# Performance work log

Measured on AMD Instinct MI355X. Metric: run time of the kernel, lower is better.

The kernel has to match this reference:

```python
import jax, jax.numpy as jnp
import numpy as np

B, S, E, H, FF = 4, 2048, 512, 8, 2048
DH = E // H
EPS = 1e-6


def setup_inputs() -> dict:
    key = jax.random.key(0)
    ks = jax.random.split(key, 16)
    sc = lambda fan_in: 1.0 / np.sqrt(fan_in)
    inp = {
        "x": jax.random.normal(ks[0], (B, S, E), dtype=jnp.float32),
        "src_mask": jnp.ones((B, 1, 1, S), dtype=jnp.int32),
        # attention projections, stored [in, out]
        "wq": jax.random.uniform(ks[1], (E, E), minval=-sc(E), maxval=sc(E)),
        "bq": jnp.zeros((E,), jnp.float32),
        "wk": jax.random.uniform(ks[2], (E, E), minval=-sc(E), maxval=sc(E)),
        "bk": jnp.zeros((E,), jnp.float32),
        "wv": jax.random.uniform(ks[3], (E, E), minval=-sc(E), maxval=sc(E)),
        "bv": jnp.zeros((E,), jnp.float32),
        "wo": jax.random.uniform(ks[4], (E, E), minval=-sc(E), maxval=sc(E)),
        "bo": jnp.zeros((E,), jnp.float32),
        # feed-forward
        "w1": jax.random.uniform(ks[5], (E, FF), minval=-sc(E), maxval=sc(E)),
        "b1": jnp.zeros((FF,), jnp.float32),
        "w2": jax.random.uniform(ks[6], (FF, E), minval=-sc(FF), maxval=sc(FF)),
        "b2": jnp.zeros((E,), jnp.float32),
        # addNormLayer scalar params (alpha init 1, bias init 0)
        "alpha1": jnp.ones((1,), jnp.float32),
        "beta1": jnp.zeros((1,), jnp.float32),
        "alpha2": jnp.ones((1,), jnp.float32),
        "beta2": jnp.zeros((1,), jnp.float32),
    }
    return inp


def _norm(x, alpha, beta):
    # matches torch: mean + unbiased std (ddof=1), eps added to std
    mean = jnp.mean(x, axis=-1, keepdims=True)
    std = jnp.std(x, axis=-1, keepdims=True, ddof=1)
    return alpha * (x - mean) / (std + EPS) + beta


def reference(x, src_mask, wq, bq, wk, bk, wv, bv, wo, bo,
              w1, b1, w2, b2, alpha1, beta1, alpha2, beta2):
    # --- residual 1: pre-norm self-attention ---
    n = _norm(x, alpha1, beta1)  # [B,S,E]
    q = (n @ wq + bq).reshape(B, S, H, DH).transpose(0, 2, 1, 3)  # [B,H,S,DH]
    k = (n @ wk + bk).reshape(B, S, H, DH).transpose(0, 2, 1, 3)
    v = (n @ wv + bv).reshape(B, S, H, DH).transpose(0, 2, 1, 3)
    scores = jnp.einsum('bhqd,bhkd->bhqk', q, k) / np.sqrt(DH)  # [B,H,S,S]
    scores = jnp.where(src_mask == 0, -1e9, scores)
    attn = jax.nn.softmax(scores, axis=-1)
    ctx = jnp.einsum('bhqk,bhkd->bhqd', attn, v)  # [B,H,S,DH]
    ctx = ctx.transpose(0, 2, 1, 3).reshape(B, S, E)
    x = x + (ctx @ wo + bo)
    # --- residual 2: pre-norm FFN ---
    n2 = _norm(x, alpha2, beta2)
    ff = jax.nn.relu(n2 @ w1 + b1) @ w2 + b2
    return x + ff
```

## Files before the change

### kernel.cpp

```cpp
#include <hip/hip_runtime.h>

typedef __bf16 bfrag __attribute__((ext_vector_type(8)));
typedef float f32x4 __attribute__((ext_vector_type(4)));
typedef unsigned short us8 __attribute__((ext_vector_type(8)));

__device__ __forceinline__ float bf2f(unsigned short s) {
  unsigned u = ((unsigned)s) << 16;
  float f;
  __builtin_memcpy(&f, &u, 4);
  return f;
}
__device__ __forceinline__ unsigned short f2bf(float f) {
  unsigned u;
  __builtin_memcpy(&u, &f, 4);
  u += 0x7fffu + ((u >> 16) & 1u);
  return (unsigned short)(u >> 16);
}
__device__ __forceinline__ float rdf(const void* p, size_t i, int isf) {
  return isf ? ((const float*)p)[i] : bf2f(((const unsigned short*)p)[i]);
}
__device__ __forceinline__ void gld16(const unsigned short* g, unsigned short* l) {
  __builtin_amdgcn_global_load_lds(
      (const __attribute__((address_space(1))) unsigned int*)g,
      (__attribute__((address_space(3))) unsigned int*)l, 16, 0, 0);
}

template <int XMODE>
__device__ void norm_unit(const void* xin, const void* alpha, const void* beta,
                          unsigned short* out, int isf, int u) {
  constexpr int E = 512;
  int xf = XMODE ? 1 : isf;
  int tid = threadIdx.x;
  int wave = tid >> 6, lane = tid & 63;
  size_t tok = (size_t)u * 4 + wave;
  float v[8];
  if (xf) {
    const float* xp = (const float*)xin + tok * E + lane * 8;
    float4 a0 = *(const float4*)xp;
    float4 a1 = *(const float4*)(xp + 4);
    v[0] = a0.x; v[1] = a0.y; v[2] = a0.z; v[3] = a0.w;
    v[4] = a1.x; v[5] = a1.y; v[6] = a1.z; v[7] = a1.w;
  } else {
    us8 uu = *(const us8*)((const unsigned short*)xin + tok * E + lane * 8);
#pragma unroll
    for (int j = 0; j < 8; j++) v[j] = bf2f(uu[j]);
  }
  float s = 0.f, sq = 0.f;
#pragma unroll
  for (int j = 0; j < 8; j++) { s += v[j]; sq += v[j] * v[j]; }
#pragma unroll
  for (int off = 1; off < 64; off <<= 1) {
    s += __shfl_xor(s, off, 64);
    sq += __shfl_xor(sq, off, 64);
  }
  float mean = s * (1.0f / 512.0f);
  float var = fmaxf((sq - 512.0f * mean * mean) * (1.0f / 511.0f), 0.0f);
  float inv = rdf(alpha, 0, isf) / (sqrtf(var) + 1e-6f);
  float be = rdf(beta, 0, isf);
  us8 ov;
#pragma unroll
  for (int j = 0; j < 8; j++) ov[j] = f2bf((v[j] - mean) * inv + be);
  *(us8*)(out + tok * E + lane * 8) = ov;
}

__global__ __launch_bounds__(256) void setup_k(
    const unsigned short* __restrict__ x16,
    const void* wq, const void* wk, const void* wv, const void* wo,
    const void* w1, const void* w2,
    unsigned short* wqkvT, unsigned short* woT,
    unsigned short* w1T, unsigned short* w2T,
    const void* bq, const void* bk, const void* bv, const void* bo,
    const void* b1, const void* b2, float* __restrict__ bcat,
    const void* alpha1, const void* beta1, unsigned short* __restrict__ n1,
    int* __restrict__ flag) {
  __shared__ unsigned short tile[32][33];
  __shared__ int s_cnt;
  int tid = threadIdx.x;
  int bid = blockIdx.x;
  if (tid == 0) s_cnt = 0;
  __syncthreads();
  {
    int c = 0;
    for (int i = tid; i < 4096; i += 256) {
      unsigned short s = x16[2 * i];
      int e = (s >> 7) & 0xFF;
      if (e > 0xC2 || (e != 0 && e < 0x3D)) c++;
    }
    atomicAdd(&s_cnt, c);
  }
  __syncthreads();
  const int isf = (s_cnt > 256) ? 1 : 0;
  if (bid == 0 && tid == 0) flag[0] = isf;

  if (bid >= 3090) {
    norm_unit<0>(x16, alpha1, beta1, n1, isf, bid - 3090);
    return;
  }
  if (bid >= 3072) {
    int i = (bid - 3072) * 256 + tid;
    if (i < 4608) {
      float v;
      if (i < 512) v = rdf(bq, i, isf);
      else if (i < 1024) v = rdf(bk, i - 512, isf);
      else if (i < 1536) v = rdf(bv, i - 1024, isf);
      else if (i < 2048) v = rdf(bo, i - 1536, isf);
      else if (i < 4096) v = rdf(b1, i - 2048, isf);
      else v = rdf(b2, i - 4096, isf);
      bcat[i] = v;
    }
    return;
  }
  const void* W;
  unsigned short* Wt;
  int K, N, t;
  if (bid < 1024) {
    K = 512; N = 512; t = bid & 255;
    if (bid < 256) { W = wq; Wt = wqkvT; }
    else if (bid < 512) { W = wk; Wt = wqkvT + 262144; }
    else if (bid < 768) { W = wv; Wt = wqkvT + 524288; }
    else { W = wo; Wt = woT; }
  } else if (bid < 2048) {
    W = w1; Wt = w1T; K = 512; N = 2048; t = bid - 1024;
  } else {
    W = w2; Wt = w2T; K = 2048; N = 512; t = bid - 2048;
  }
  int nx = N >> 5;
  int n0 = (t % nx) * 32, k0 = (t / nx) * 32;
#pragma unroll
  for (int i = 0; i < 4; i++) {
    int e = tid + i * 256;
    int r = e >> 5, c = e & 31;
    tile[r][c] = f2bf(rdf(W, (size_t)(k0 + r) * N + n0 + c, isf));
  }
  __syncthreads();
#pragma unroll
  for (int i = 0; i < 4; i++) {
    int e = tid + i * 256;
    int r = e >> 5, c = e & 31;
    Wt[(size_t)(n0 + r) * K + k0 + c] = tile[c][r];
  }
}

__global__ __launch_bounds__(256) void vtrans_k(
    const unsigned short* __restrict__ qkb, unsigned short* __restrict__ vbt) {
  __shared__ unsigned short tile[32][33];
  int tid = threadIdx.x;
  int u = blockIdx.x;
  int s0 = (u & 63) * 32;
  int d0 = ((u >> 6) & 1) * 32;
  int bh = u >> 7, b = bh >> 3, h = bh & 7;
#pragma unroll
  for (int i = 0; i < 4; i++) {
    int e = tid + i * 256;
    int r = e >> 5, c = e & 31;
    tile[r][c] = qkb[((size_t)b * 2048 + s0 + r) * 1536 + 1024 + h * 64 + d0 + c];
  }
  __syncthreads();
#pragma unroll
  for (int i = 0; i < 4; i++) {
    int e = tid + i * 256;
    int r = e >> 5, c = e & 31;
    vbt[((size_t)bh * 64 + d0 + r) * 2048 + s0 + c] = tile[c][r];
  }
}

__global__ __launch_bounds__(256) void norm2_k(
    const void* __restrict__ xin, const void* __restrict__ alpha,
    const void* __restrict__ beta, unsigned short* __restrict__ out,
    const int* __restrict__ flag) {
  norm_unit<1>(xin, alpha, beta, out, flag[0], blockIdx.x);
}

template <int TN, int RES, int OUTM, int RELU>
__global__ __launch_bounds__(256, 3) void gemm2_k(
    const unsigned short* __restrict__ A,
    const unsigned short* __restrict__ Bt,
    const float* __restrict__ bias,
    const void* __restrict__ res,
    void* __restrict__ outp,
    int N, int K, const int* __restrict__ flag) {
  constexpr int MT = (TN == 128) ? 4 : 2;
  constexpr int BROWS = TN / 4;
  __shared__ alignas(16) unsigned short As[128 * 64];
  __shared__ alignas(16) unsigned short Bs[TN * 64];
  int isf = flag[0];
  int outf32 = (OUTM == 1) || (OUTM == 2 && isf);
  int tid = threadIdx.x;
  int wave = tid >> 6, lane = tid & 63;
  int quad = lane >> 4, l16 = lane & 15, l7 = l16 & 7;
  int wm = (TN == 128) ? (wave >> 1) : wave;
  int wn = (TN == 128) ? (wave & 1) : 0;
  size_t m0 = (size_t)blockIdx.x * 128;
  size_t n0 = (size_t)blockIdx.y * TN;

  int lrow = lane >> 3;
  int gcol = 8 * ((lane & 7) ^ lrow);

  const unsigned short* ag = A + (m0 + wave * 32 + lrow) * K + gcol;
  const unsigned short* bg = Bt + (n0 + wave * BROWS + lrow) * K + gcol;
  unsigned short* asl = &As[(wave * 32) * 64];
  unsigned short* bsl = &Bs[(wave * BROWS) * 64];

  f32x4 acc[MT][4];
#pragma unroll
  for (int i = 0; i < MT; i++)
#pragma unroll
    for (int j = 0; j < 4; j++) acc[i][j] = {0.f, 0.f, 0.f, 0.f};

  for (int k0 = 0; k0 < K; k0 += 64) {
    __syncthreads();
#pragma unroll
    for (int c = 0; c < 4; c++)
      gld16(ag + (size_t)(8 * c) * K + k0, asl + (8 * c) * 64);
#pragma unroll
    for (int c = 0; c < BROWS / 8; c++)
      gld16(bg + (size_t)(8 * c) * K + k0, bsl + (8 * c) * 64);
    __syncthreads();
#pragma unroll
    for (int ko = 0; ko < 2; ko++) {
      int slot = ((4 * ko + quad) ^ l7) * 8;
      bfrag af[MT], bf[4];
#pragma unroll
      for (int i = 0; i < MT; i++)
        af[i] = *(const bfrag*)&As[(wm * (MT * 16) + i * 16 + l16) * 64 + slot];
#pragma unroll
      for (int j = 0; j < 4; j++)
        bf[j] = *(const bfrag*)&Bs[(wn * 64 + j * 16 + l16) * 64 + slot];
#pragma unroll
      for (int i = 0; i < MT; i++)
#pragma unroll
        for (int j = 0; j < 4; j++)
          acc[i][j] = __builtin_amdgcn_mfma_f32_16x16x32_bf16(af[i], bf[j], acc[i][j], 0, 0, 0);
    }
  }
#pragma unroll
  for (int j = 0; j < 4; j++) {
    size_t n = n0 + wn * 64 + j * 16 + l16;
    float bv = bias[n];
#pragma unroll
    for (int i = 0; i < MT; i++) {
#pragma unroll
      for (int r = 0; r < 4; r++) {
        size_t m = m0 + wm * (MT * 16) + i * 16 + quad * 4 + r;
        float vv = acc[i][j][r] + bv;
        if (RELU) vv = fmaxf(vv, 0.0f);
        if (RES == 1) vv += rdf(res, m * N + n, isf);
        else if (RES == 2) vv += ((const float*)res)[m * N + n];
        if (outf32) ((float*)outp)[m * N + n] = vv;
        else ((unsigned short*)outp)[m * N + n] = f2bf(vv);
      }
    }
  }
}

__global__ __launch_bounds__(256) void attn_k(
    const unsigned short* __restrict__ qkb,
    const unsigned short* __restrict__ vbt,
    const int* __restrict__ mask,
    unsigned short* __restrict__ ctx) {
  constexpr int S = 2048;
  __shared__ alignas(16) unsigned short Kt[64][72];
  __shared__ alignas(16) unsigned short Vt[64][72];
  __shared__ alignas(16) unsigned short Pl[4][16][68];
  __shared__ float mskf[64];
  int tid = threadIdx.x, wave = tid >> 6, lane = tid & 63;
  int quad = lane >> 4, l16 = lane & 15;
  int q0 = blockIdx.x * 64;
  int bh = blockIdx.y, b = bh >> 3, h = bh & 7;
  size_t rowbase = (size_t)b * S;

  bfrag qf0, qf1;
  {
    const unsigned short* qp =
        qkb + (rowbase + q0 + wave * 16 + l16) * 1536 + h * 64 + quad * 8;
    qf0 = *(const bfrag*)qp;
    qf1 = *(const bfrag*)(qp + 32);
  }
  f32x4 o[4] = {{0, 0, 0, 0}, {0, 0, 0, 0}, {0, 0, 0, 0}, {0, 0, 0, 0}};
  float l_i[4] = {0.f, 0.f, 0.f, 0.f};

  int srow = tid >> 2;
  int c0 = (tid & 3) * 8;
  const unsigned short* kbase = qkb + 512 + h * 64;
  const unsigned short* vrow = vbt + ((size_t)bh * 64 + srow) * S;
  const float SC = 0.18033688f;

  for (int kt = 0; kt < S; kt += 64) {
    __syncthreads();
    {
      const unsigned short* kp = kbase + (rowbase + kt + srow) * 1536;
      *(uint4*)&Kt[srow][c0]      = *(const uint4*)(kp + c0);
      *(uint4*)&Kt[srow][c0 + 32] = *(const uint4*)(kp + c0 + 32);
      *(uint4*)&Vt[srow][c0]      = *(const uint4*)(vrow + kt + c0);
      *(uint4*)&Vt[srow][c0 + 32] = *(const uint4*)(vrow + kt + c0 + 32);
    }
    if (tid < 64) mskf[tid] = mask[rowbase + kt + tid] ? 0.0f : -1e5f;
    __syncthreads();

    float pr[4][4];
#pragma unroll
    for (int nt = 0; nt < 4; nt++) {
      f32x4 s = {0, 0, 0, 0};
      bfrag k0f = *(const bfrag*)&Kt[nt * 16 + l16][quad * 8];
      bfrag k1f = *(const bfrag*)&Kt[nt * 16 + l16][32 + quad * 8];
      s = __builtin_amdgcn_mfma_f32_16x16x32_bf16(qf0, k0f, s, 0, 0, 0);
      s = __builtin_amdgcn_mfma_f32_16x16x32_bf16(qf1, k1f, s, 0, 0, 0);
      float mb = mskf[nt * 16 + l16];
#pragma unroll
      for (int r = 0; r < 4; r++) {
        float p = __builtin_amdgcn_exp2f(fminf(fmaf(s[r], SC, mb), 50.0f));
        pr[nt][r] = p;
        unsigned u;
        __builtin_memcpy(&u, &p, 4);
        Pl[wave][quad * 4 + r][nt * 16 + l16] = (unsigned short)(u >> 16);
      }
    }
#pragma unroll
    for (int r = 0; r < 4; r++)
      l_i[r] += (pr[0][r] + pr[1][r]) + (pr[2][r] + pr[3][r]);
    bfrag pa0 = *(const bfrag*)&Pl[wave][l16][quad * 8];
    bfrag pa1 = *(const bfrag*)&Pl[wave][l16][32 + quad * 8];
#pragma unroll
    for (int dt = 0; dt < 4; dt++) {
      bfrag v0 = *(const bfrag*)&Vt[dt * 16 + l16][quad * 8];
      bfrag v1 = *(const bfrag*)&Vt[dt * 16 + l16][32 + quad * 8];
      o[dt] = __builtin_amdgcn_mfma_f32_16x16x32_bf16(pa0, v0, o[dt], 0, 0, 0);
      o[dt] = __builtin_amdgcn_mfma_f32_16x16x32_bf16(pa1, v1, o[dt], 0, 0, 0);
    }
  }
#pragma unroll
  for (int r = 0; r < 4; r++) {
#pragma unroll
    for (int off = 1; off < 16; off <<= 1) l_i[r] += __shfl_xor(l_i[r], off, 64);
    l_i[r] = 1.0f / fmaxf(l_i[r], 1e-30f);
  }
#pragma unroll
  for (int dt = 0; dt < 4; dt++) {
#pragma unroll
    for (int r = 0; r < 4; r++) {
      size_t qrow = rowbase + q0 + wave * 16 + quad * 4 + r;
      ctx[qrow * 512 + h * 64 + dt * 16 + l16] = f2bf(o[dt][r] * l_i[r]);
    }
  }
}

extern "C" void kernel_launch(void* const* d_in, const int* in_sizes, int n_in,
                              void* d_out, int out_size, void* d_ws, size_t ws_size,
                              hipStream_t stream) {
  const unsigned short* x = (const unsigned short*)d_in[0];
  const int* mask         = (const int*)d_in[1];
  const void* wq = d_in[2];  const void* bq = d_in[3];
  const void* wk = d_in[4];  const void* bk = d_in[5];
  const void* wv = d_in[6];  const void* bv = d_in[7];
  const void* wo = d_in[8];  const void* bo = d_in[9];
  const void* w1 = d_in[10]; const void* b1 = d_in[11];
  const void* w2 = d_in[12]; const void* b2 = d_in[13];
  const void* alpha1 = d_in[14]; const void* beta1 = d_in[15];
  const void* alpha2 = d_in[16]; const void* beta2 = d_in[17];

  char* ws = (char*)d_ws;
  int* flag            = (int*)(ws + 0);
  unsigned short* wqkvT= (unsigned short*)(ws + 65536);
  unsigned short* woT  = (unsigned short*)(ws + 1638400);
  unsigned short* w1T  = (unsigned short*)(ws + 2162688);
  unsigned short* w2T  = (unsigned short*)(ws + 4259840);
  float*          bcat = (float*)         (ws + 6356992);
  float*          x1   = (float*)         (ws + 6422528);
  unsigned short* n1   = (unsigned short*)(ws + 23199744);
  unsigned short* qkb  = (unsigned short*)(ws + 31588352);
  unsigned short* vbt  = (unsigned short*)(ws + 56754176);
  unsigned short* ff1  = qkb;

  dim3 blk(256);

  setup_k<<<5138, blk, 0, stream>>>(x, wq, wk, wv, wo, w1, w2,
                                    wqkvT, woT, w1T, w2T,
                                    bq, bk, bv, bo, b1, b2, bcat,
                                    alpha1, beta1, n1, flag);
  gemm2_k<128, 0, 0, 0><<<dim3(64, 12), blk, 0, stream>>>(n1, wqkvT, bcat, nullptr, qkb, 1536, 512, flag);
  vtrans_k<<<4096, blk, 0, stream>>>(qkb, vbt);
  attn_k<<<dim3(32, 32), blk, 0, stream>>>(qkb, vbt, mask, n1);
  gemm2_k<64, 1, 1, 0><<<dim3(64, 8), blk, 0, stream>>>(n1, woT, bcat + 1536, (const void*)x, x1, 512, 512, flag);
  norm2_k<<<2048, blk, 0, stream>>>(x1, alpha2, beta2, n1, flag);
  gemm2_k<128, 0, 0, 1><<<dim3(64, 16), blk, 0, stream>>>(n1, w1T, bcat + 2048, nullptr, ff1, 2048, 512, flag);
  gemm2_k<64, 2, 2, 0><<<dim3(64, 8), blk, 0, stream>>>(ff1, w2T, bcat + 4096, x1, d_out, 512, 2048, flag);
}
```

Before: 310.5 us.

## Rewrite attention with 32x32 MFMA, swizzled direct-to-LDS loads, register P transfer

```diff
diff --git a/kernel.cpp b/kernel.cpp
--- a/kernel.cpp
+++ b/kernel.cpp
@@ -2,7 +2,10 @@
 
 typedef __bf16 bfrag __attribute__((ext_vector_type(8)));
 typedef float f32x4 __attribute__((ext_vector_type(4)));
+typedef float f32x16 __attribute__((ext_vector_type(16)));
 typedef unsigned short us8 __attribute__((ext_vector_type(8)));
+typedef unsigned int u32x2 __attribute__((ext_vector_type(2)));
+typedef unsigned int u32x4 __attribute__((ext_vector_type(4)));
 
 __device__ __forceinline__ float bf2f(unsigned short s) {
   unsigned u = ((unsigned)s) << 16;
@@ -23,6 +26,11 @@
   __builtin_amdgcn_global_load_lds(
       (const __attribute__((address_space(1))) unsigned int*)g,
       (__attribute__((address_space(3))) unsigned int*)l, 16, 0, 0);
+}
+__device__ __forceinline__ unsigned cvtpk_bf16(float a, float b) {
+  unsigned d;
+  asm("v_cvt_pk_bf16_f32 %0, %1, %2" : "=v"(d) : "v"(a), "v"(b));
+  return d;
 }
 
 template <int XMODE>
@@ -253,93 +261,120 @@
   }
 }
 
-__global__ __launch_bounds__(256) void attn_k(
+__global__ __launch_bounds__(256, 2) void attn_k(
     const unsigned short* __restrict__ qkb,
     const unsigned short* __restrict__ vbt,
     const int* __restrict__ mask,
     unsigned short* __restrict__ ctx) {
   constexpr int S = 2048;
-  __shared__ alignas(16) unsigned short Kt[64][72];
-  __shared__ alignas(16) unsigned short Vt[64][72];
-  __shared__ alignas(16) unsigned short Pl[4][16][68];
-  __shared__ float mskf[64];
+  __shared__ alignas(16) unsigned short Kt[64 * 64];
+  __shared__ alignas(16) unsigned short Vt[64 * 64];
+  __shared__ alignas(16) float mskf[64];
+  __shared__ float linv[128];
   int tid = threadIdx.x, wave = tid >> 6, lane = tid & 63;
-  int quad = lane >> 4, l16 = lane & 15;
-  int q0 = blockIdx.x * 64;
+  int l32 = lane & 31, hi = lane >> 5;
+  int q0 = blockIdx.x * 128;
   int bh = blockIdx.y, b = bh >> 3, h = bh & 7;
   size_t rowbase = (size_t)b * S;
-
-  bfrag qf0, qf1;
+  const float SC = 0.18033688f;
+
+  bfrag qf[4];
   {
     const unsigned short* qp =
-        qkb + (rowbase + q0 + wave * 16 + l16) * 1536 + h * 64 + quad * 8;
-    qf0 = *(const bfrag*)qp;
-    qf1 = *(const bfrag*)(qp + 32);
-  }
-  f32x4 o[4] = {{0, 0, 0, 0}, {0, 0, 0, 0}, {0, 0, 0, 0}, {0, 0, 0, 0}};
-  float l_i[4] = {0.f, 0.f, 0.f, 0.f};
-
-  int srow = tid >> 2;
-  int c0 = (tid & 3) * 8;
-  const unsigned short* kbase = qkb + 512 + h * 64;
-  const unsigned short* vrow = vbt + ((size_t)bh * 64 + srow) * S;
-  const float SC = 0.18033688f;
+        qkb + (rowbase + q0 + wave * 32 + l32) * 1536 + h * 64 + hi * 8;
+#pragma unroll
+    for (int ds = 0; ds < 4; ds++) qf[ds] = *(const bfrag*)(qp + ds * 16);
+  }
+
+  int srow_l = lane >> 3;
+  int sc = lane & 7;
+  const unsigned short* kgb = qkb + 512 + h * 64;
+  const unsigned short* vgb = vbt + (size_t)bh * 64 * S;
+
+  f32x16 o[2];
+#pragma unroll
+  for (int i = 0; i < 16; i++) { o[0][i] = 0.f; o[1][i] = 0.f; }
+  float l_i = 0.f;
 
   for (int kt = 0; kt < S; kt += 64) {
     __syncthreads();
     {
-      const unsigned short* kp = kbase + (rowbase + kt + srow) * 1536;
-      *(uint4*)&Kt[srow][c0]      = *(const uint4*)(kp + c0);
-      *(uint4*)&Kt[srow][c0 + 32] = *(const uint4*)(kp + c0 + 32);
-      *(uint4*)&Vt[srow][c0]      = *(const uint4*)(vrow + kt + c0);
-      *(uint4*)&Vt[srow][c0 + 32] = *(const uint4*)(vrow + kt + c0 + 32);
+#pragma unroll
+      for (int i = 0; i < 2; i++) {
+        int r = wave * 16 + i * 8 + srow_l;
+        gld16(kgb + (rowbase + kt + r) * 1536 + (size_t)((sc ^ (r & 7)) * 8),
+              &Kt[(wave * 16 + i * 8) * 64]);
+        gld16(vgb + (size_t)r * S + kt + (size_t)((sc ^ (r & 7)) * 8),
+              &Vt[(wave * 16 + i * 8) * 64]);
+      }
     }
     if (tid < 64) mskf[tid] = mask[rowbase + kt + tid] ? 0.0f : -1e5f;
     __syncthreads();
 
-    float pr[4][4];
-#pragma unroll
-    for (int nt = 0; nt < 4; nt++) {
-      f32x4 s = {0, 0, 0, 0};
-      bfrag k0f = *(const bfrag*)&Kt[nt * 16 + l16][quad * 8];
-      bfrag k1f = *(const bfrag*)&Kt[nt * 16 + l16][32 + quad * 8];
-      s = __builtin_amdgcn_mfma_f32_16x16x32_bf16(qf0, k0f, s, 0, 0, 0);
-      s = __builtin_amdgcn_mfma_f32_16x16x32_bf16(qf1, k1f, s, 0, 0, 0);
-      float mb = mskf[nt * 16 + l16];
-#pragma unroll
-      for (int r = 0; r < 4; r++) {
-        float p = __builtin_amdgcn_exp2f(fminf(fmaf(s[r], SC, mb), 50.0f));
-        pr[nt][r] = p;
-        unsigned u;
-        __builtin_memcpy(&u, &p, 4);
-        Pl[wave][quad * 4 + r][nt * 16 + l16] = (unsigned short)(u >> 16);
+    f32x16 pacc[2];
+#pragma unroll
+    for (int t = 0; t < 2; t++)
+#pragma unroll
+      for (int i = 0; i < 16; i++) pacc[t][i] = 0.f;
+#pragma unroll
+    for (int t = 0; t < 2; t++) {
+      int r = t * 32 + l32;
+#pragma unroll
+      for (int ds = 0; ds < 4; ds++) {
+        int phys = ((2 * ds + hi) ^ (r & 7)) * 8;
+        bfrag kf = *(const bfrag*)&Kt[r * 64 + phys];
+        pacc[t] = __builtin_amdgcn_mfma_f32_32x32x16_bf16(kf, qf[ds], pacc[t], 0, 0, 0);
       }
     }
-#pragma unroll
-    for (int r = 0; r < 4; r++)
-      l_i[r] += (pr[0][r] + pr[1][r]) + (pr[2][r] + pr[3][r]);
-    bfrag pa0 = *(const bfrag*)&Pl[wave][l16][quad * 8];
-    bfrag pa1 = *(const bfrag*)&Pl[wave][l16][32 + quad * 8];
-#pragma unroll
-    for (int dt = 0; dt < 4; dt++) {
-      bfrag v0 = *(const bfrag*)&Vt[dt * 16 + l16][quad * 8];
-      bfrag v1 = *(const bfrag*)&Vt[dt * 16 + l16][32 + quad * 8];
-      o[dt] = __builtin_amdgcn_mfma_f32_16x16x32_bf16(pa0, v0, o[dt], 0, 0, 0);
-      o[dt] = __builtin_amdgcn_mfma_f32_16x16x32_bf16(pa1, v1, o[dt], 0, 0, 0);
-    }
-  }
-#pragma unroll
-  for (int r = 0; r < 4; r++) {
-#pragma unroll
-    for (int off = 1; off < 16; off <<= 1) l_i[r] += __shfl_xor(l_i[r], off, 64);
-    l_i[r] = 1.0f / fmaxf(l_i[r], 1e-30f);
-  }
-#pragma unroll
-  for (int dt = 0; dt < 4; dt++) {
-#pragma unroll
-    for (int r = 0; r < 4; r++) {
-      size_t qrow = rowbase + q0 + wave * 16 + quad * 4 + r;
-      ctx[qrow * 512 + h * 64 + dt * 16 + l16] = f2bf(o[dt][r] * l_i[r]);
+
+    unsigned pb[2][8];
+#pragma unroll
+    for (int t = 0; t < 2; t++) {
+#pragma unroll
+      for (int g = 0; g < 4; g++) {
+        float4 m4 = *(const float4*)&mskf[t * 32 + g * 8 + hi * 4];
+        float p0 = __builtin_amdgcn_exp2f(fminf(fmaf(pacc[t][g * 4 + 0], SC, m4.x), 50.0f));
+        float p1 = __builtin_amdgcn_exp2f(fminf(fmaf(pacc[t][g * 4 + 1], SC, m4.y), 50.0f));
+        float p2 = __builtin_amdgcn_exp2f(fminf(fmaf(pacc[t][g * 4 + 2], SC, m4.z), 50.0f));
+        float p3 = __builtin_amdgcn_exp2f(fminf(fmaf(pacc[t][g * 4 + 3], SC, m4.w), 50.0f));
+        l_i += (p0 + p1) + (p2 + p3);
+        pb[t][g * 2] = cvtpk_bf16(p0, p1);
+        pb[t][g * 2 + 1] = cvtpk_bf16(p2, p3);
+      }
+    }
+
+#pragma unroll
+    for (int ks = 0; ks < 4; ks++) {
+      int t = ks >> 1, e = ks & 1;
+      u32x2 sA = __builtin_amdgcn_permlane32_swap(pb[t][4 * e + 0], pb[t][4 * e + 2], false, false);
+      u32x2 sB = __builtin_amdgcn_permlane32_swap(pb[t][4 * e + 1], pb[t][4 * e + 3], false, false);
+      u32x4 pw = {sA.x, sB.x, sA.y, sB.y};
+      bfrag pf = __builtin_bit_cast(bfrag, pw);
+#pragma unroll
+      for (int dt = 0; dt < 2; dt++) {
+        int r = dt * 32 + l32;
+        int phys = ((2 * ks + hi) ^ (r & 7)) * 8;
+        bfrag vf = *(const bfrag*)&Vt[r * 64 + phys];
+        o[dt] = __builtin_amdgcn_mfma_f32_32x32x16_bf16(pf, vf, o[dt], 0, 0, 0);
+      }
+    }
+  }
+
+  {
+    unsigned lu = __builtin_bit_cast(unsigned, l_i);
+    u32x2 lr = __builtin_amdgcn_permlane32_swap(lu, lu, false, false);
+    float l_tot = __builtin_bit_cast(float, lr.x) + __builtin_bit_cast(float, lr.y);
+    if (lane < 32) linv[wave * 32 + l32] = 1.0f / fmaxf(l_tot, 1e-30f);
+  }
+  __syncthreads();
+#pragma unroll
+  for (int dt = 0; dt < 2; dt++) {
+#pragma unroll
+    for (int reg = 0; reg < 16; reg++) {
+      int ql = (reg & 3) + 8 * (reg >> 2) + 4 * hi;
+      size_t qrow = rowbase + q0 + wave * 32 + ql;
+      ctx[qrow * 512 + h * 64 + dt * 32 + l32] =
+          f2bf(o[dt][reg] * linv[wave * 32 + ql]);
     }
   }
 }
@@ -379,7 +414,7 @@
                                     alpha1, beta1, n1, flag);
   gemm2_k<128, 0, 0, 0><<<dim3(64, 12), blk, 0, stream>>>(n1, wqkvT, bcat, nullptr, qkb, 1536, 512, flag);
   vtrans_k<<<4096, blk, 0, stream>>>(qkb, vbt);
-  attn_k<<<dim3(32, 32), blk, 0, stream>>>(qkb, vbt, mask, n1);
+  attn_k<<<dim3(16, 32), blk, 0, stream>>>(qkb, vbt, mask, n1);
   gemm2_k<64, 1, 1, 0><<<dim3(64, 8), blk, 0, stream>>>(n1, woT, bcat + 1536, (const void*)x, x1, 512, 512, flag);
   norm2_k<<<2048, blk, 0, stream>>>(x1, alpha2, beta2, n1, flag);
   gemm2_k<128, 0, 0, 1><<<dim3(64, 16), blk, 0, stream>>>(n1, w1T, bcat + 2048, nullptr, ff1, 2048, 512, flag);
```

New measurement: 286.2 us. 7.8% less time.
